# Kernel tuning notes

Measured on AMD Instinct MI355X. Metric: run time of the kernel, lower is better.

The kernel has to match this reference:

```python
import jax, jax.numpy as jnp
import numpy as np

BETA = 0.5
LAMBDA = 0.5
EPS = 1e-24


def setup_inputs() -> dict:
    key = jax.random.key(0)
    k1, k2 = jax.random.split(key)
    seq = jax.random.normal(k1, (32, 512, 128), dtype=jnp.float32)
    fism_items = jax.random.normal(k2, (32, 2048, 128), dtype=jnp.float32)
    return {"seq": seq, "fism_items": fism_items}


def reference(seq, fism_items):
    # scores: [B, L, N]
    w = jnp.einsum('bld,bnd->bln', seq, fism_items)
    w_shift = w - jnp.max(w, axis=-1, keepdims=True)
    exp_w = jnp.exp(w_shift)
    exp_sum = jnp.sum(exp_w, axis=-1, keepdims=True)
    if BETA != 1.0:
        exp_sum = jnp.power(exp_sum, jnp.float32(BETA))
    att = exp_w / (exp_sum + EPS)  # power-normalized softmax
    att_vecs = jnp.einsum('bln,bnd->bld', att, fism_items)
    if LAMBDA < 1:
        return seq * (1.0 - LAMBDA) + seq * att_vecs * LAMBDA
    return seq * att_vecs
```

## Files before the change

kernel.cpp:

```cpp
#include <hip/hip_runtime.h>
#include <hip/hip_bf16.h>
#include <math.h>

typedef _Float16 half8  __attribute__((ext_vector_type(8)));
typedef _Float16 half4v __attribute__((ext_vector_type(4)));
typedef __fp16   fp16x2 __attribute__((ext_vector_type(2)));
typedef float    f32x4  __attribute__((ext_vector_type(4)));
typedef float    f32x16 __attribute__((ext_vector_type(16)));
typedef int      i32x2v __attribute__((ext_vector_type(2)));

#define DDIM 128
#define LQ   512
#define NKV  2048
#define NB   32
#define NIT  16

union U32H2 { unsigned u; fp16x2 h; };
union PW    { unsigned u[4]; half8 h; };

__device__ __forceinline__ float xmax64(float v) {
  i32x2v r = __builtin_amdgcn_permlane32_swap(__float_as_int(v), __float_as_int(v), false, false);
  return fmaxf(__int_as_float(r[0]), __int_as_float(r[1]));
}
__device__ __forceinline__ float xsum64(float v) {
  i32x2v r = __builtin_amdgcn_permlane32_swap(__float_as_int(v), __float_as_int(v), false, false);
  return __int_as_float(r[0]) + __int_as_float(r[1]);
}

__device__ __forceinline__ void dma16(const void* g, void* l) {
  __builtin_amdgcn_global_load_lds(
      (const __attribute__((address_space(1))) unsigned int*)g,
      (__attribute__((address_space(3))) unsigned int*)l, 16, 0, 0);
}

__global__ __launch_bounds__(256)
void prep(const float* __restrict__ fism, _Float16* __restrict__ K16,
          _Float16* __restrict__ VT16)
{
  __shared__ _Float16 T[64 * DDIM];
  const int tid = threadIdx.x;
  const int bb  = blockIdx.x >> 5;
  const int kv0 = (blockIdx.x & 31) * 64;
  {
    const int r  = tid >> 2;
    const int cq = tid & 3;
    const float* src = fism + ((size_t)(bb*NKV + kv0 + r) * DDIM + cq*32);
    _Float16*    kd  = K16  + ((size_t)(bb*NKV + kv0 + r) * DDIM + cq*32);
    float4 v[8];
    #pragma unroll
    for (int k = 0; k < 8; ++k) v[k] = ((const float4*)src)[k];
    _Float16 h[32];
    #pragma unroll
    for (int k = 0; k < 8; ++k) {
      h[4*k+0] = (_Float16)v[k].x; h[4*k+1] = (_Float16)v[k].y;
      h[4*k+2] = (_Float16)v[k].z; h[4*k+3] = (_Float16)v[k].w;
    }
    #pragma unroll
    for (int k = 0; k < 4; ++k) ((half8*)kd)[k] = *(half8*)&h[8*k];
    #pragma unroll
    for (int j = 0; j < 32; ++j) {
      const int d = cq*32 + j;
      T[d*64 + (((r>>3) ^ (d&7))<<3) + (r&7)] = h[j];
    }
  }
  __syncthreads();
  {
    const int d  = tid >> 1;
    const int kh = tid & 1;
    _Float16* vd = VT16 + ((size_t)(bb*DDIM + d) * NKV + kv0 + kh*32);
    #pragma unroll
    for (int u = 0; u < 4; ++u) {
      const int k8 = kh*4 + u;
      ((half8*)vd)[u] = *(half8*)&T[d*64 + ((k8 ^ (d&7))<<3)];
    }
  }
}

__global__ __launch_bounds__(256, 2)
void gattn(const float* __restrict__ seq, const _Float16* __restrict__ K16,
           const _Float16* __restrict__ VT16, float* __restrict__ out)
{
  __shared__ __align__(16) unsigned char POOL[65536];
  __shared__ float stats[2][32][4];

  const int tid  = threadIdx.x;
  const int lane = tid & 63;
  const int wv   = tid >> 6;
  const int qg   = wv & 1;
  const int kvh  = wv >> 1;
  const int l31  = lane & 31;
  const int hi   = lane >> 5;

  const int swz = (blockIdx.x & 7) * 32 + (blockIdx.x >> 3);
  const int b   = swz >> 3;
  const int qb  = (swz & 7) * 64;

  const float* seqB = seq + (size_t)b * LQ * DDIM;
  float*       outB = out + (size_t)b * LQ * DDIM;
  const _Float16* K16b  = K16  + (size_t)b * NKV * DDIM;
  const _Float16* VT16b = VT16 + (size_t)b * DDIM * NKV;

  half8 qf[8];
  {
    const int qrow = qb + qg * 32 + l31;
    #pragma unroll
    for (int c = 0; c < 8; ++c) {
      const float* p = seqB + (size_t)qrow * DDIM + c * 16 + hi * 8;
      float4 a  = *(const float4*)p;
      float4 b2 = *(const float4*)(p + 4);
      half8 h;
      h[0]=(_Float16)a.x;  h[1]=(_Float16)a.y;  h[2]=(_Float16)a.z;  h[3]=(_Float16)a.w;
      h[4]=(_Float16)b2.x; h[5]=(_Float16)b2.y; h[6]=(_Float16)b2.z; h[7]=(_Float16)b2.w;
      qf[c] = h;
    }
  }

  const bool isK = (wv < 2);
  const int  hst = isK ? wv : (wv - 2);
  int off[16];
  #pragma unroll
  for (int i = 0; i < 16; ++i) {
    const int unit = i*64 + lane;
    const int r16 = unit >> 4, sp = unit & 15;
    const int s = sp ^ (r16 & 15);
    if (isK) {
      off[i] = r16*128 + s*8;
    } else {
      const int d = r16*2 + (s >> 3);
      off[i] = d*2048 + (s & 7)*8;
    }
  }
  const _Float16* sb0 = isK ? (K16b + (size_t)hst*1024*128) : (VT16b + hst*1024);
  const int tstr  = isK ? 8192 : 64;
  const int lbase = (isK ? 0 : 32768) + hst*16384;

  auto stage = [&](int tt) {
    const _Float16* s0 = sb0 + (size_t)tt * tstr;
    #pragma unroll
    for (int i = 0; i < 16; ++i)
      dma16(s0 + off[i], &POOL[lbase + i*1024]);
  };

  f32x16 acc[4];
  #pragma unroll
  for (int dt = 0; dt < 4; ++dt)
    #pragma unroll
    for (int i = 0; i < 16; ++i) acc[dt][i] = 0.f;

  float m_run = -INFINITY, tmax = -INFINITY, S_run = 0.f;

  stage(0);

  for (int t = 0; t < NIT; ++t) {
    __syncthreads();

    f32x16 sv[2];
    __builtin_amdgcn_s_setprio(1);
    #pragma unroll
    for (int ns = 0; ns < 2; ++ns) {
      f32x16 x;
      #pragma unroll
      for (int i = 0; i < 16; ++i) x[i] = 0.f;
      const int krow = ns*32 + l31;
      const int kb_  = kvh*16384 + krow*256;
      const int ksw  = krow & 15;
      #pragma unroll
      for (int c = 0; c < 8; ++c) {
        const int u = 2*c + hi;
        half8 ka = *(const half8*)&POOL[kb_ + ((u ^ ksw) << 4)];
        x = __builtin_amdgcn_mfma_f32_32x32x16_f16(ka, qf[c], x, 0, 0, 0);
      }
      sv[ns] = x;
    }
    __builtin_amdgcn_s_setprio(0);

    __syncthreads();
    if (isK && t + 1 < NIT) stage(t + 1);

    float mx[16];
    #pragma unroll
    for (int i = 0; i < 16; ++i) mx[i] = fmaxf(sv[0][i], sv[1][i]);
    #pragma unroll
    for (int st = 8; st > 0; st >>= 1)
      #pragma unroll
      for (int i = 0; i < st; ++i) mx[i] = fmaxf(mx[i], mx[i+st]);
    const float cmax = xmax64(mx[0]);
    tmax = fmaxf(tmax, cmax);
    if (__any(cmax > m_run + 8.f)) {
      const float mn = fmaxf(m_run, cmax);
      const float sc = __expf(m_run - mn);
      S_run *= sc;
      m_run = mn;
      #pragma unroll
      for (int dt = 0; dt < 4; ++dt) acc[dt] *= sc;
    }
    float ts[16];
    #pragma unroll
    for (int i = 0; i < 16; ++i) {
      const float p0 = __expf(sv[0][i] - m_run);
      const float p1 = __expf(sv[1][i] - m_run);
      sv[0][i] = p0; sv[1][i] = p1;
      ts[i] = p0 + p1;
    }
    #pragma unroll
    for (int st = 8; st > 0; st >>= 1)
      #pragma unroll
      for (int i = 0; i < st; ++i) ts[i] += ts[i+st];
    S_run += xsum64(ts[0]);

    PW pw[4];
    #pragma unroll
    for (int nss = 0; nss < 2; ++nss)
      #pragma unroll
      for (int b0 = 0; b0 < 2; ++b0) {
        U32H2 t0, t1, t2, t3;
        t0.h = __builtin_amdgcn_cvt_pkrtz(sv[nss][8*b0+0], sv[nss][8*b0+1]);
        t1.h = __builtin_amdgcn_cvt_pkrtz(sv[nss][8*b0+2], sv[nss][8*b0+3]);
        t2.h = __builtin_amdgcn_cvt_pkrtz(sv[nss][8*b0+4], sv[nss][8*b0+5]);
        t3.h = __builtin_amdgcn_cvt_pkrtz(sv[nss][8*b0+6], sv[nss][8*b0+7]);
        i32x2v r0 = __builtin_amdgcn_permlane32_swap((int)t0.u, (int)t2.u, false, false);
        i32x2v r1 = __builtin_amdgcn_permlane32_swap((int)t1.u, (int)t3.u, false, false);
        const int kb = 2*nss + b0;
        pw[kb].u[0] = (unsigned)r0[0];
        pw[kb].u[1] = (unsigned)r1[0];
        pw[kb].u[2] = (unsigned)r0[1];
        pw[kb].u[3] = (unsigned)r1[1];
      }

    __builtin_amdgcn_s_setprio(1);
    #pragma unroll
    for (int dt = 0; dt < 4; ++dt) {
      const int d    = dt*32 + l31;
      const int dRow = d >> 1, dSub = d & 1;
      const int vsw  = dRow & 15;
      const int vb   = 32768 + kvh*16384 + dRow*256;
      #pragma unroll
      for (int kb = 0; kb < 4; ++kb) {
        const int u = dSub*8 + kb*2 + hi;
        half8 vtf = *(const half8*)&POOL[vb + ((u ^ vsw) << 4)];
        acc[dt] = __builtin_amdgcn_mfma_f32_32x32x16_f16(vtf, pw[kb].h, acc[dt], 0, 0, 0);
      }
    }
    __builtin_amdgcn_s_setprio(0);

    __syncthreads();
    if (!isK && t + 1 < NIT) stage(t + 1);
  }

  __syncthreads();

  if (kvh == 1) {
    float* base = (float*)&POOL[qg * 16384];
    #pragma unroll
    for (int dt = 0; dt < 4; ++dt)
      #pragma unroll
      for (int rg = 0; rg < 4; ++rg) {
        const int j = dt*4 + rg;
        f32x4 v = {acc[dt][4*rg+0], acc[dt][4*rg+1], acc[dt][4*rg+2], acc[dt][4*rg+3]};
        *(f32x4*)&base[lane*64 + ((j ^ (lane & 15)) << 2)] = v;
      }
    if (lane < 32) {
      stats[qg][lane][0] = m_run;
      stats[qg][lane][1] = S_run;
      stats[qg][lane][2] = tmax;
    }
  }
  __syncthreads();

  if (kvh == 0) {
    const float m1 = stats[qg][l31][0];
    const float S1 = stats[qg][l31][1];
    const float t1 = stats[qg][l31][2];
    const float M2 = fmaxf(m_run, m1);
    const float e0 = __expf(m_run - M2), e1 = __expf(m1 - M2);
    const float S  = S_run * e0 + S1 * e1;
    const float T  = fmaxf(tmax, t1);
    const float fs = __expf(0.5f * (M2 - T)) * rsqrtf(S);

    const float* base = (const float*)&POOL[qg * 16384];
    const int qrw = qb + qg*32 + l31;
    #pragma unroll
    for (int dt = 0; dt < 4; ++dt) {
      #pragma unroll
      for (int rg = 0; rg < 4; ++rg) {
        const int j = dt*4 + rg;
        const f32x4 pj = *(const f32x4*)&base[lane*64 + ((j ^ (lane & 15)) << 2)];
        f32x4 av;
        #pragma unroll
        for (int i = 0; i < 4; ++i)
          av[i] = (acc[dt][4*rg+i] * e0 + pj[i] * e1) * fs;
        const int d0 = dt*32 + rg*8 + hi*4;
        const float4 s = *(const float4*)&seqB[(size_t)qrw * DDIM + d0];
        float4 o;
        o.x = 0.5f * s.x * (1.f + av[0]);
        o.y = 0.5f * s.y * (1.f + av[1]);
        o.z = 0.5f * s.z * (1.f + av[2]);
        o.w = 0.5f * s.w * (1.f + av[3]);
        *(float4*)&outB[(size_t)qrw * DDIM + d0] = o;
      }
    }
  }
}

__global__ __launch_bounds__(512, 2)
void gattn_fb(const float* __restrict__ seq, const float* __restrict__ fism,
              float* __restrict__ out)
{
  const int tid  = threadIdx.x;
  const int lane = tid & 63;
  const int wv   = tid >> 6;
  const int wq   = wv & 1;
  const int kvq  = wv >> 1;
  const int l31  = lane & 31;
  const int hi   = lane >> 5;

  const int swz = (blockIdx.x & 7) * 32 + (blockIdx.x >> 3);
  const int b   = swz >> 3;
  const int qb  = (swz & 7) * 64;

  const float* seqB = seq  + (size_t)b * LQ * DDIM;
  const float* fisB = fism + (size_t)b * NKV * DDIM;
  float*       outB = out  + (size_t)b * LQ * DDIM;

  __shared__ _Float16 Ksh[4][64 * DDIM];
  __shared__ _Float16 VTsh[4][(DDIM/2) * 128];
  __shared__ float    stats[4][2][32][3];

  half8 qf[8];
  {
    const int qrow = qb + wq * 32 + l31;
    #pragma unroll
    for (int c = 0; c < 8; ++c) {
      const float* p = seqB + (size_t)qrow * DDIM + c * 16 + hi * 8;
      float4 a  = *(const float4*)p;
      float4 b2 = *(const float4*)(p + 4);
      half8 h;
      h[0]=(_Float16)a.x;  h[1]=(_Float16)a.y;  h[2]=(_Float16)a.z;  h[3]=(_Float16)a.w;
      h[4]=(_Float16)b2.x; h[5]=(_Float16)b2.y; h[6]=(_Float16)b2.z; h[7]=(_Float16)b2.w;
      qf[c] = h;
    }
  }

  const int sp   = tid >> 3;
  const int dgrp = tid & 7;
  const int qstg = sp >> 4;
  const int spc  = sp & 15;

  f32x16 acc[4];
  #pragma unroll
  for (int dt = 0; dt < 4; ++dt)
    #pragma unroll
    for (int i = 0; i < 16; ++i) acc[dt][i] = 0.f;

  float m_run = -INFINITY, tmax = -INFINITY, S_run = 0.f;

  auto write_stage = [&](const float4* v) {
    #pragma unroll
    for (int r = 0; r < 4; ++r) {
      const int row = 4*spc + r;
      #pragma unroll
      for (int hh = 0; hh < 2; ++hh) {
        const float4 x = v[r*4 + hh*2];
        const float4 y = v[r*4 + hh*2 + 1];
        half8 h;
        h[0]=(_Float16)x.x; h[1]=(_Float16)x.y; h[2]=(_Float16)x.z; h[3]=(_Float16)x.w;
        h[4]=(_Float16)y.x; h[5]=(_Float16)y.y; h[6]=(_Float16)y.z; h[7]=(_Float16)y.w;
        const int idx = row*DDIM + ((dgrp*16 + hh*8) ^ (8*(row & 15)));
        *(half8*)&Ksh[qstg][idx] = h;
      }
    }
    #pragma unroll
    for (int k = 0; k < 16; ++k) {
      const int d = dgrp*16 + k;
      const int dRow = d >> 1, dSub = d & 1;
      half4v pk;
      #pragma unroll
      for (int r = 0; r < 4; ++r)
        pk[r] = (_Float16)(((const float*)&v[r*4 + (k>>2)])[k&3]);
      const int idx = dRow*128 + ((dSub*64 + 4*spc) ^ (8*(dRow & 15)));
      *(half4v*)&VTsh[qstg][idx] = pk;
    }
  };

  auto load_glb = [&](float4* v, int t) {
    const float* src = fisB + (size_t)(qstg*(NKV/4) + t*64) * DDIM;
    #pragma unroll
    for (int r = 0; r < 4; ++r)
      #pragma unroll
      for (int k = 0; k < 4; ++k)
        v[r*4+k] = *(const float4*)(src + (size_t)(4*spc + r)*DDIM + dgrp*16 + k*4);
  };

  {
    float4 stg[16];
    load_glb(stg, 0);
    write_stage(stg);
  }

  for (int t = 0; t < 8; ++t) {
    __syncthreads();
    float4 nxt[16];
    const bool have = (t + 1 < 8);
    if (have) load_glb(nxt, t + 1);

    f32x16 sv[2];
    #pragma unroll
    for (int nss = 0; nss < 2; ++nss) {
      f32x16 x;
      #pragma unroll
      for (int i = 0; i < 16; ++i) x[i] = 0.f;
      const int row = nss*32 + l31;
      const int sw  = 8*(row & 15);
      #pragma unroll
      for (int c = 0; c < 8; ++c) {
        const int idx = row*DDIM + ((c*16 + hi*8) ^ sw);
        half8 kf = *(const half8*)&Ksh[kvq][idx];
        x = __builtin_amdgcn_mfma_f32_32x32x16_f16(kf, qf[c], x, 0, 0, 0);
      }
      sv[nss] = x;
    }

    float mx[16];
    #pragma unroll
    for (int i = 0; i < 16; ++i) mx[i] = fmaxf(sv[0][i], sv[1][i]);
    #pragma unroll
    for (int st = 8; st > 0; st >>= 1)
      #pragma unroll
      for (int i = 0; i < st; ++i) mx[i] = fmaxf(mx[i], mx[i+st]);
    const float cmax = xmax64(mx[0]);
    tmax = fmaxf(tmax, cmax);
    if (__any(cmax > m_run + 8.f)) {
      const float mn = fmaxf(m_run, cmax);
      const float sc = __expf(m_run - mn);
      S_run *= sc;
      m_run = mn;
      #pragma unroll
      for (int dt = 0; dt < 4; ++dt) acc[dt] *= sc;
    }
    float ts[16];
    #pragma unroll
    for (int i = 0; i < 16; ++i) {
      const float p0 = __expf(sv[0][i] - m_run);
      const float p1 = __expf(sv[1][i] - m_run);
      sv[0][i] = p0; sv[1][i] = p1;
      ts[i] = p0 + p1;
    }
    #pragma unroll
    for (int st = 8; st > 0; st >>= 1)
      #pragma unroll
      for (int i = 0; i < st; ++i) ts[i] += ts[i+st];
    S_run += xsum64(ts[0]);

    PW pw[4];
    #pragma unroll
    for (int nss = 0; nss < 2; ++nss)
      #pragma unroll
      for (int b0 = 0; b0 < 2; ++b0) {
        U32H2 t0, t1, t2, t3;
        t0.h = __builtin_amdgcn_cvt_pkrtz(sv[nss][8*b0+0], sv[nss][8*b0+1]);
        t1.h = __builtin_amdgcn_cvt_pkrtz(sv[nss][8*b0+2], sv[nss][8*b0+3]);
        t2.h = __builtin_amdgcn_cvt_pkrtz(sv[nss][8*b0+4], sv[nss][8*b0+5]);
        t3.h = __builtin_amdgcn_cvt_pkrtz(sv[nss][8*b0+6], sv[nss][8*b0+7]);
        i32x2v r0 = __builtin_amdgcn_permlane32_swap((int)t0.u, (int)t2.u, false, false);
        i32x2v r1 = __builtin_amdgcn_permlane32_swap((int)t1.u, (int)t3.u, false, false);
        const int kb = 2*nss + b0;
        pw[kb].u[0] = (unsigned)r0[0];
        pw[kb].u[1] = (unsigned)r1[0];
        pw[kb].u[2] = (unsigned)r0[1];
        pw[kb].u[3] = (unsigned)r1[1];
      }

    #pragma unroll
    for (int dt = 0; dt < 4; ++dt) {
      const int d    = dt*32 + l31;
      const int dRow = d >> 1, dSub = d & 1;
      const int sw   = 8*(dRow & 15);
      #pragma unroll
      for (int kb = 0; kb < 4; ++kb) {
        const int idx = dRow*128 + ((dSub*64 + kb*16 + hi*8) ^ sw);
        half8 vtf = *(const half8*)&VTsh[kvq][idx];
        acc[dt] = __builtin_amdgcn_mfma_f32_32x32x16_f16(vtf, pw[kb].h, acc[dt], 0, 0, 0);
      }
    }

    __syncthreads();
    if (have) write_stage(nxt);
  }

  __syncthreads();

  float* Kf  = (float*)&Ksh[0][0];
  float* VTf = (float*)&VTsh[0][0];
  if (kvq != 0) {
    const int rgn = (kvq - 1) * 2 + wq;
    float* base = (rgn < 4) ? (Kf + rgn * 4096) : (VTf + (rgn - 4) * 4096);
    #pragma unroll
    for (int dt = 0; dt < 4; ++dt)
      #pragma unroll
      for (int rg = 0; rg < 4; ++rg) {
        f32x4 v = {acc[dt][4*rg+0], acc[dt][4*rg+1], acc[dt][4*rg+2], acc[dt][4*rg+3]};
        *(f32x4*)&base[lane*64 + (((dt*4+rg) ^ (lane & 15)) * 4)] = v;
      }
    if (lane < 32) {
      stats[kvq][wq][lane][0] = m_run;
      stats[kvq][wq][lane][1] = S_run;
      stats[kvq][wq][lane][2] = tmax;
    }
  }
  __syncthreads();

  if (kvq == 0) {
    float mj[4], Sj[4], tj[4];
    mj[0] = m_run; Sj[0] = S_run; tj[0] = tmax;
    #pragma unroll
    for (int j = 1; j < 4; ++j) {
      mj[j] = stats[j][wq][l31][0];
      Sj[j] = stats[j][wq][l31][1];
      tj[j] = stats[j][wq][l31][2];
    }
    const float M = fmaxf(fmaxf(tj[0], tj[1]), fmaxf(tj[2], tj[3]));
    float fj[4], den = 0.f;
    #pragma unroll
    for (int j = 0; j < 4; ++j) { fj[j] = __expf(mj[j] - M); den += fj[j] * Sj[j]; }
    const float rs = rsqrtf(den);
    #pragma unroll
    for (int j = 0; j < 4; ++j) fj[j] *= rs;

    const int qrow = qb + wq*32 + l31;
    #pragma unroll
    for (int dt = 0; dt < 4; ++dt) {
      #pragma unroll
      for (int rg = 0; rg < 4; ++rg) {
        f32x4 av = {acc[dt][4*rg+0], acc[dt][4*rg+1], acc[dt][4*rg+2], acc[dt][4*rg+3]};
        av *= fj[0];
        #pragma unroll
        for (int j = 1; j < 4; ++j) {
          const int rgn = (j - 1) * 2 + wq;
          const float* base = (rgn < 4) ? (Kf + rgn * 4096) : (VTf + (rgn - 4) * 4096);
          const f32x4 pj = *(const f32x4*)&base[lane*64 + (((dt*4+rg) ^ (lane & 15)) * 4)];
          av += pj * fj[j];
        }
        const int d0 = dt*32 + rg*8 + hi*4;
        const float4 s = *(const float4*)&seqB[(size_t)qrow * DDIM + d0];
        float4 o;
        o.x = 0.5f * s.x * (1.f + av[0]);
        o.y = 0.5f * s.y * (1.f + av[1]);
        o.z = 0.5f * s.z * (1.f + av[2]);
        o.w = 0.5f * s.w * (1.f + av[3]);
        *(float4*)&outB[(size_t)qrow * DDIM + d0] = o;
      }
    }
  }
}

extern "C" void kernel_launch(void* const* d_in, const int* in_sizes, int n_in,
                              void* d_out, int out_size, void* d_ws, size_t ws_size,
                              hipStream_t stream) {
  const float* seq  = (const float*)d_in[0];
  const float* fism = (const float*)d_in[1];
  float* out = (float*)d_out;
  if (ws_size >= 33554432ull) {
    _Float16* K16  = (_Float16*)d_ws;
    _Float16* VT16 = K16 + (size_t)NB * NKV * DDIM;
    prep<<<dim3(1024), dim3(256), 0, stream>>>(fism, K16, VT16);
    gattn<<<dim3(256), dim3(256), 0, stream>>>(seq, K16, VT16, out);
  } else {
    gattn_fb<<<dim3(256), dim3(512), 0, stream>>>(seq, fism, out);
  }
}
```

Baseline: 60.75 us.

## Load MFMA-fragment-ordered K/V directly to registers, split KV across four waves

The prep kernel now writes K and V in the exact per-lane MFMA fragment order, so the attention kernel loads them straight from global memory into registers instead of staging through LDS with DMA and block barriers. Each block handles 32 queries, with its four waves each covering a quarter of the KV range, and the grid doubles to 512 blocks. The four partial softmax states are merged at the end through shared memory. This removes the per-iteration __syncthreads and LDS traffic, at the cost of much higher register pressure from holding K and V fragments in registers, and each block now re-reads K/V for only 32 queries.

```diff
diff --git a/kernel.cpp b/kernel.cpp
--- a/kernel.cpp
+++ b/kernel.cpp
@@ -13,7 +13,7 @@
 #define LQ   512
 #define NKV  2048
 #define NB   32
-#define NIT  16
+#define NIT  8
 
 union U32H2 { unsigned u; fp16x2 h; };
 union PW    { unsigned u[4]; half8 h; };
@@ -27,25 +27,19 @@
   return __int_as_float(r[0]) + __int_as_float(r[1]);
 }
 
-__device__ __forceinline__ void dma16(const void* g, void* l) {
-  __builtin_amdgcn_global_load_lds(
-      (const __attribute__((address_space(1))) unsigned int*)g,
-      (__attribute__((address_space(3))) unsigned int*)l, 16, 0, 0);
-}
-
 __global__ __launch_bounds__(256)
-void prep(const float* __restrict__ fism, _Float16* __restrict__ K16,
-          _Float16* __restrict__ VT16)
+void prep(const float* __restrict__ fism, _Float16* __restrict__ KF,
+          _Float16* __restrict__ VF)
 {
   __shared__ _Float16 T[64 * DDIM];
   const int tid = threadIdx.x;
   const int bb  = blockIdx.x >> 5;
-  const int kv0 = (blockIdx.x & 31) * 64;
+  const int idx = blockIdx.x & 31;
+  const int kv0 = idx * 64;
   {
     const int r  = tid >> 2;
     const int cq = tid & 3;
     const float* src = fism + ((size_t)(bb*NKV + kv0 + r) * DDIM + cq*32);
-    _Float16*    kd  = K16  + ((size_t)(bb*NKV + kv0 + r) * DDIM + cq*32);
     float4 v[8];
     #pragma unroll
     for (int k = 0; k < 8; ++k) v[k] = ((const float4*)src)[k];
@@ -55,8 +49,15 @@
       h[4*k+0] = (_Float16)v[k].x; h[4*k+1] = (_Float16)v[k].y;
       h[4*k+2] = (_Float16)v[k].z; h[4*k+3] = (_Float16)v[k].w;
     }
-    #pragma unroll
-    for (int k = 0; k < 4; ++k) ((half8*)kd)[k] = *(half8*)&h[8*k];
+    const size_t kfb = (size_t)(bb*32 + idx) * 8192;
+    const int ns = r >> 5, l31r = r & 31;
+    #pragma unroll
+    for (int g = 0; g < 4; ++g) {
+      const int c   = cq*2 + (g >> 1);
+      const int hig = g & 1;
+      const int unit = (ns*8 + c)*64 + hig*32 + l31r;
+      *(half8*)&KF[kfb + (size_t)unit*8] = *(half8*)&h[(g>>1)*16 + hig*8];
+    }
     #pragma unroll
     for (int j = 0; j < 32; ++j) {
       const int d = cq*32 + j;
@@ -65,81 +66,53 @@
   }
   __syncthreads();
   {
-    const int d  = tid >> 1;
-    const int kh = tid & 1;
-    _Float16* vd = VT16 + ((size_t)(bb*DDIM + d) * NKV + kv0 + kh*32);
-    #pragma unroll
-    for (int u = 0; u < 4; ++u) {
-      const int k8 = kh*4 + u;
-      ((half8*)vd)[u] = *(half8*)&T[d*64 + ((k8 ^ (d&7))<<3)];
+    const size_t vfb = (size_t)(bb*32 + idx) * 8192;
+    #pragma unroll
+    for (int j = 0; j < 4; ++j) {
+      const int u  = tid*4 + j;
+      const int dt = u >> 8, kb = (u >> 6) & 3, l = u & 63;
+      const int d  = dt*32 + (l & 31);
+      const int kv8 = kb*2 + (l >> 5);
+      *(half8*)&VF[vfb + (size_t)u*8] = *(half8*)&T[d*64 + ((kv8 ^ (d & 7)) << 3)];
     }
   }
 }
 
 __global__ __launch_bounds__(256, 2)
-void gattn(const float* __restrict__ seq, const _Float16* __restrict__ K16,
-           const _Float16* __restrict__ VT16, float* __restrict__ out)
+void gattn(const float* __restrict__ seq, const _Float16* __restrict__ KF,
+           const _Float16* __restrict__ VF, float* __restrict__ out)
 {
-  __shared__ __align__(16) unsigned char POOL[65536];
-  __shared__ float stats[2][32][4];
+  __shared__ __align__(16) unsigned char POOL[49152];
+  __shared__ float stats[4][32][4];
 
   const int tid  = threadIdx.x;
   const int lane = tid & 63;
-  const int wv   = tid >> 6;
-  const int qg   = wv & 1;
-  const int kvh  = wv >> 1;
+  const int kvh  = tid >> 6;
   const int l31  = lane & 31;
   const int hi   = lane >> 5;
 
-  const int swz = (blockIdx.x & 7) * 32 + (blockIdx.x >> 3);
-  const int b   = swz >> 3;
-  const int qb  = (swz & 7) * 64;
+  const int swzb = (blockIdx.x & 7) * 64 + (blockIdx.x >> 3);
+  const int b    = swzb >> 4;
+  const int qb   = (swzb & 15) * 32;
 
   const float* seqB = seq + (size_t)b * LQ * DDIM;
   float*       outB = out + (size_t)b * LQ * DDIM;
-  const _Float16* K16b  = K16  + (size_t)b * NKV * DDIM;
-  const _Float16* VT16b = VT16 + (size_t)b * DDIM * NKV;
-
-  half8 qf[8];
-  {
-    const int qrow = qb + qg * 32 + l31;
-    #pragma unroll
-    for (int c = 0; c < 8; ++c) {
-      const float* p = seqB + (size_t)qrow * DDIM + c * 16 + hi * 8;
-      float4 a  = *(const float4*)p;
-      float4 b2 = *(const float4*)(p + 4);
-      half8 h;
-      h[0]=(_Float16)a.x;  h[1]=(_Float16)a.y;  h[2]=(_Float16)a.z;  h[3]=(_Float16)a.w;
-      h[4]=(_Float16)b2.x; h[5]=(_Float16)b2.y; h[6]=(_Float16)b2.z; h[7]=(_Float16)b2.w;
-      qf[c] = h;
-    }
-  }
-
-  const bool isK = (wv < 2);
-  const int  hst = isK ? wv : (wv - 2);
-  int off[16];
+
   #pragma unroll
-  for (int i = 0; i < 16; ++i) {
-    const int unit = i*64 + lane;
-    const int r16 = unit >> 4, sp = unit & 15;
-    const int s = sp ^ (r16 & 15);
-    if (isK) {
-      off[i] = r16*128 + s*8;
-    } else {
-      const int d = r16*2 + (s >> 3);
-      off[i] = d*2048 + (s & 7)*8;
-    }
-  }
-  const _Float16* sb0 = isK ? (K16b + (size_t)hst*1024*128) : (VT16b + hst*1024);
-  const int tstr  = isK ? 8192 : 64;
-  const int lbase = (isK ? 0 : 32768) + hst*16384;
-
-  auto stage = [&](int tt) {
-    const _Float16* s0 = sb0 + (size_t)tt * tstr;
-    #pragma unroll
-    for (int i = 0; i < 16; ++i)
-      dma16(s0 + off[i], &POOL[lbase + i*1024]);
-  };
+  for (int j = 0; j < 2; ++j) {
+    const int u = tid*2 + j;
+    const int c = u >> 6, l = u & 63;
+    const float* qs = seqB + (size_t)(qb + (l & 31)) * DDIM + c*16 + (l >> 5)*8;
+    float4 a  = ((const float4*)qs)[0];
+    float4 b2 = ((const float4*)qs)[1];
+    _Float16 hq[8];
+    hq[0]=(_Float16)a.x;  hq[1]=(_Float16)a.y;  hq[2]=(_Float16)a.z;  hq[3]=(_Float16)a.w;
+    hq[4]=(_Float16)b2.x; hq[5]=(_Float16)b2.y; hq[6]=(_Float16)b2.z; hq[7]=(_Float16)b2.w;
+    *(half8*)&POOL[u*16] = *(half8*)hq;
+  }
+  __syncthreads();
+
+  const int cb = b*32 + kvh*8;
 
   f32x16 acc[4];
   #pragma unroll
@@ -149,10 +122,22 @@
 
   float m_run = -INFINITY, tmax = -INFINITY, S_run = 0.f;
 
-  stage(0);
-
+  half8 kf[16], vfr0[8], vfr1[8];
+  {
+    const _Float16* KFc = KF + (size_t)cb * 8192;
+    #pragma unroll
+    for (int i = 0; i < 16; ++i) kf[i] = *(const half8*)(KFc + (size_t)(i*64 + lane)*8);
+  }
+
+  #pragma unroll
   for (int t = 0; t < NIT; ++t) {
-    __syncthreads();
+    const _Float16* VFc = VF + (size_t)(cb + t) * 8192;
+    #pragma unroll
+    for (int i = 0; i < 8; ++i) vfr0[i] = *(const half8*)(VFc + (size_t)(i*64 + lane)*8);
+
+    half8 qa[8];
+    #pragma unroll
+    for (int c = 0; c < 8; ++c) qa[c] = *(const half8*)&POOL[(c*64 + lane)*16];
 
     f32x16 sv[2];
     __builtin_amdgcn_s_setprio(1);
@@ -161,21 +146,20 @@
       f32x16 x;
       #pragma unroll
       for (int i = 0; i < 16; ++i) x[i] = 0.f;
-      const int krow = ns*32 + l31;
-      const int kb_  = kvh*16384 + krow*256;
-      const int ksw  = krow & 15;
-      #pragma unroll
-      for (int c = 0; c < 8; ++c) {
-        const int u = 2*c + hi;
-        half8 ka = *(const half8*)&POOL[kb_ + ((u ^ ksw) << 4)];
-        x = __builtin_amdgcn_mfma_f32_32x32x16_f16(ka, qf[c], x, 0, 0, 0);
-      }
+      #pragma unroll
+      for (int c = 0; c < 8; ++c)
+        x = __builtin_amdgcn_mfma_f32_32x32x16_f16(kf[ns*8+c], qa[c], x, 0, 0, 0);
       sv[ns] = x;
     }
     __builtin_amdgcn_s_setprio(0);
 
-    __syncthreads();
-    if (isK && t + 1 < NIT) stage(t + 1);
+    if (t + 1 < NIT) {
+      const _Float16* KFn = KF + (size_t)(cb + t + 1) * 8192;
+      #pragma unroll
+      for (int i = 0; i < 16; ++i) kf[i] = *(const half8*)(KFn + (size_t)(i*64 + lane)*8);
+    }
+    #pragma unroll
+    for (int i = 0; i < 8; ++i) vfr1[i] = *(const half8*)(VFc + (size_t)((8+i)*64 + lane)*8);
 
     float mx[16];
     #pragma unroll
@@ -230,27 +214,18 @@
     __builtin_amdgcn_s_setprio(1);
     #pragma unroll
     for (int dt = 0; dt < 4; ++dt) {
-      const int d    = dt*32 + l31;
-      const int dRow = d >> 1, dSub = d & 1;
-      const int vsw  = dRow & 15;
-      const int vb   = 32768 + kvh*16384 + dRow*256;
       #pragma unroll
       for (int kb = 0; kb < 4; ++kb) {
-        const int u = dSub*8 + kb*2 + hi;
-        half8 vtf = *(const half8*)&POOL[vb + ((u ^ vsw) << 4)];
-        acc[dt] = __builtin_amdgcn_mfma_f32_32x32x16_f16(vtf, pw[kb].h, acc[dt], 0, 0, 0);
+        const half8 v = (dt < 2) ? vfr0[dt*4 + kb] : vfr1[(dt-2)*4 + kb];
+        acc[dt] = __builtin_amdgcn_mfma_f32_32x32x16_f16(v, pw[kb].h, acc[dt], 0, 0, 0);
       }
     }
     __builtin_amdgcn_s_setprio(0);
-
-    __syncthreads();
-    if (!isK && t + 1 < NIT) stage(t + 1);
   }
 
   __syncthreads();
-
-  if (kvh == 1) {
-    float* base = (float*)&POOL[qg * 16384];
+  if (kvh != 0) {
+    float* base = (float*)&POOL[(kvh - 1) * 16384];
     #pragma unroll
     for (int dt = 0; dt < 4; ++dt)
       #pragma unroll
@@ -260,35 +235,46 @@
         *(f32x4*)&base[lane*64 + ((j ^ (lane & 15)) << 2)] = v;
       }
     if (lane < 32) {
-      stats[qg][lane][0] = m_run;
-      stats[qg][lane][1] = S_run;
-      stats[qg][lane][2] = tmax;
+      stats[kvh][lane][0] = m_run;
+      stats[kvh][lane][1] = S_run;
+      stats[kvh][lane][2] = tmax;
     }
   }
   __syncthreads();
 
   if (kvh == 0) {
-    const float m1 = stats[qg][l31][0];
-    const float S1 = stats[qg][l31][1];
-    const float t1 = stats[qg][l31][2];
-    const float M2 = fmaxf(m_run, m1);
-    const float e0 = __expf(m_run - M2), e1 = __expf(m1 - M2);
-    const float S  = S_run * e0 + S1 * e1;
-    const float T  = fmaxf(tmax, t1);
-    const float fs = __expf(0.5f * (M2 - T)) * rsqrtf(S);
-
-    const float* base = (const float*)&POOL[qg * 16384];
-    const int qrw = qb + qg*32 + l31;
+    float mj[4], Sj[4], tj[4];
+    mj[0] = m_run; Sj[0] = S_run; tj[0] = tmax;
+    #pragma unroll
+    for (int j = 1; j < 4; ++j) {
+      mj[j] = stats[j][l31][0];
+      Sj[j] = stats[j][l31][1];
+      tj[j] = stats[j][l31][2];
+    }
+    const float M = fmaxf(fmaxf(mj[0], mj[1]), fmaxf(mj[2], mj[3]));
+    const float T = fmaxf(fmaxf(tj[0], tj[1]), fmaxf(tj[2], tj[3]));
+    float ej[4], den = 0.f;
+    #pragma unroll
+    for (int j = 0; j < 4; ++j) { ej[j] = __expf(mj[j] - M); den += ej[j] * Sj[j]; }
+    const float fs = __expf(0.5f * (M - T)) * rsqrtf(den);
+    #pragma unroll
+    for (int j = 0; j < 4; ++j) ej[j] *= fs;
+
+    const int qrw = qb + l31;
     #pragma unroll
     for (int dt = 0; dt < 4; ++dt) {
       #pragma unroll
       for (int rg = 0; rg < 4; ++rg) {
-        const int j = dt*4 + rg;
-        const f32x4 pj = *(const f32x4*)&base[lane*64 + ((j ^ (lane & 15)) << 2)];
+        const int jj = dt*4 + rg;
         f32x4 av;
         #pragma unroll
-        for (int i = 0; i < 4; ++i)
-          av[i] = (acc[dt][4*rg+i] * e0 + pj[i] * e1) * fs;
+        for (int i = 0; i < 4; ++i) av[i] = acc[dt][4*rg+i] * ej[0];
+        #pragma unroll
+        for (int j = 1; j < 4; ++j) {
+          const float* base = (const float*)&POOL[(j - 1) * 16384];
+          const f32x4 pj = *(const f32x4*)&base[lane*64 + ((jj ^ (lane & 15)) << 2)];
+          av += pj * ej[j];
+        }
         const int d0 = dt*32 + rg*8 + hi*4;
         const float4 s = *(const float4*)&seqB[(size_t)qrw * DDIM + d0];
         float4 o;
@@ -560,10 +546,10 @@
   const float* fism = (const float*)d_in[1];
   float* out = (float*)d_out;
   if (ws_size >= 33554432ull) {
-    _Float16* K16  = (_Float16*)d_ws;
-    _Float16* VT16 = K16 + (size_t)NB * NKV * DDIM;
-    prep<<<dim3(1024), dim3(256), 0, stream>>>(fism, K16, VT16);
-    gattn<<<dim3(256), dim3(256), 0, stream>>>(seq, K16, VT16, out);
+    _Float16* KF = (_Float16*)d_ws;
+    _Float16* VF = KF + (size_t)NB * NKV * DDIM;
+    prep<<<dim3(1024), dim3(256), 0, stream>>>(fism, KF, VF);
+    gattn<<<dim3(512), dim3(256), 0, stream>>>(seq, KF, VF, out);
   } else {
     gattn_fb<<<dim3(256), dim3(512), 0, stream>>>(seq, fism, out);
   }
```

New measurement: 62.54 us. 2.9% more time.

## Pre-swizzle K/V into MFMA fragment order and double-buffer LDS stages

Applied to the files above, without the earlier changes.

The prep kernel now writes K and V^T in exactly the per-lane MFMA fragment order, so the attention kernel's DMA loads become contiguous and its LDS reads need no XOR swizzle arithmetic. LDS grows to 128 KB to double-buffer each KV tile, so the next stage is issued right after a single barrier per iteration instead of two barriers with split K/V staging. In exchange occupancy drops from two blocks per CU to one, and the linear fragment layout may cause LDS bank conflicts on the ds_read side.

```diff
diff --git a/kernel.cpp b/kernel.cpp
--- a/kernel.cpp
+++ b/kernel.cpp
@@ -34,18 +34,18 @@
 }
 
 __global__ __launch_bounds__(256)
-void prep(const float* __restrict__ fism, _Float16* __restrict__ K16,
-          _Float16* __restrict__ VT16)
+void prep(const float* __restrict__ fism, _Float16* __restrict__ KF,
+          _Float16* __restrict__ VF)
 {
   __shared__ _Float16 T[64 * DDIM];
   const int tid = threadIdx.x;
   const int bb  = blockIdx.x >> 5;
-  const int kv0 = (blockIdx.x & 31) * 64;
+  const int idx = blockIdx.x & 31;
+  const int kv0 = idx * 64;
   {
     const int r  = tid >> 2;
     const int cq = tid & 3;
     const float* src = fism + ((size_t)(bb*NKV + kv0 + r) * DDIM + cq*32);
-    _Float16*    kd  = K16  + ((size_t)(bb*NKV + kv0 + r) * DDIM + cq*32);
     float4 v[8];
     #pragma unroll
     for (int k = 0; k < 8; ++k) v[k] = ((const float4*)src)[k];
@@ -55,8 +55,15 @@
       h[4*k+0] = (_Float16)v[k].x; h[4*k+1] = (_Float16)v[k].y;
       h[4*k+2] = (_Float16)v[k].z; h[4*k+3] = (_Float16)v[k].w;
     }
-    #pragma unroll
-    for (int k = 0; k < 4; ++k) ((half8*)kd)[k] = *(half8*)&h[8*k];
+    const size_t kfb = (size_t)(bb*32 + idx) * 8192;
+    const int ns = r >> 5, l31r = r & 31;
+    #pragma unroll
+    for (int g = 0; g < 4; ++g) {
+      const int c   = cq*2 + (g >> 1);
+      const int hig = g & 1;
+      const int unit = (ns*8 + c)*64 + hig*32 + l31r;
+      *(half8*)&KF[kfb + (size_t)unit*8] = *(half8*)&h[(g>>1)*16 + hig*8];
+    }
     #pragma unroll
     for (int j = 0; j < 32; ++j) {
       const int d = cq*32 + j;
@@ -65,22 +72,23 @@
   }
   __syncthreads();
   {
-    const int d  = tid >> 1;
-    const int kh = tid & 1;
-    _Float16* vd = VT16 + ((size_t)(bb*DDIM + d) * NKV + kv0 + kh*32);
-    #pragma unroll
-    for (int u = 0; u < 4; ++u) {
-      const int k8 = kh*4 + u;
-      ((half8*)vd)[u] = *(half8*)&T[d*64 + ((k8 ^ (d&7))<<3)];
-    }
-  }
-}
-
-__global__ __launch_bounds__(256, 2)
-void gattn(const float* __restrict__ seq, const _Float16* __restrict__ K16,
-           const _Float16* __restrict__ VT16, float* __restrict__ out)
+    const size_t vfb = (size_t)(bb*32 + idx) * 8192;
+    #pragma unroll
+    for (int j = 0; j < 4; ++j) {
+      const int u  = tid*4 + j;
+      const int dt = u >> 8, kb = (u >> 6) & 3, l = u & 63;
+      const int d  = dt*32 + (l & 31);
+      const int kv8 = kb*2 + (l >> 5);
+      *(half8*)&VF[vfb + (size_t)u*8] = *(half8*)&T[d*64 + ((kv8 ^ (d & 7)) << 3)];
+    }
+  }
+}
+
+__global__ __launch_bounds__(256, 1)
+void gattn(const float* __restrict__ seq, const _Float16* __restrict__ KF,
+           const _Float16* __restrict__ VF, float* __restrict__ out)
 {
-  __shared__ __align__(16) unsigned char POOL[65536];
+  __shared__ __align__(16) unsigned char POOL[131072];
   __shared__ float stats[2][32][4];
 
   const int tid  = threadIdx.x;
@@ -97,8 +105,23 @@
 
   const float* seqB = seq + (size_t)b * LQ * DDIM;
   float*       outB = out + (size_t)b * LQ * DDIM;
-  const _Float16* K16b  = K16  + (size_t)b * NKV * DDIM;
-  const _Float16* VT16b = VT16 + (size_t)b * DDIM * NKV;
+  const _Float16* KFb = KF + (size_t)b * 32 * 8192;
+  const _Float16* VFb = VF + (size_t)b * 32 * 8192;
+
+  const bool isK = (wv < 2);
+  const int  hst = isK ? wv : (wv - 2);
+  const _Float16* sbase = (isK ? KFb : VFb) + (size_t)hst * 16 * 8192;
+  const int lgrp = (isK ? 0 : 65536) + hst * 32768;
+
+  auto stage = [&](int tt) {
+    const _Float16* s0 = sbase + (size_t)tt * 8192;
+    const int l0 = lgrp + (tt & 1) * 16384;
+    #pragma unroll
+    for (int i = 0; i < 16; ++i)
+      dma16(s0 + (size_t)(i*64 + lane)*8, &POOL[l0 + i*1024]);
+  };
+
+  stage(0);
 
   half8 qf[8];
   {
@@ -115,32 +138,6 @@
     }
   }
 
-  const bool isK = (wv < 2);
-  const int  hst = isK ? wv : (wv - 2);
-  int off[16];
-  #pragma unroll
-  for (int i = 0; i < 16; ++i) {
-    const int unit = i*64 + lane;
-    const int r16 = unit >> 4, sp = unit & 15;
-    const int s = sp ^ (r16 & 15);
-    if (isK) {
-      off[i] = r16*128 + s*8;
-    } else {
-      const int d = r16*2 + (s >> 3);
-      off[i] = d*2048 + (s & 7)*8;
-    }
-  }
-  const _Float16* sb0 = isK ? (K16b + (size_t)hst*1024*128) : (VT16b + hst*1024);
-  const int tstr  = isK ? 8192 : 64;
-  const int lbase = (isK ? 0 : 32768) + hst*16384;
-
-  auto stage = [&](int tt) {
-    const _Float16* s0 = sb0 + (size_t)tt * tstr;
-    #pragma unroll
-    for (int i = 0; i < 16; ++i)
-      dma16(s0 + off[i], &POOL[lbase + i*1024]);
-  };
-
   f32x16 acc[4];
   #pragma unroll
   for (int dt = 0; dt < 4; ++dt)
@@ -149,10 +146,12 @@
 
   float m_run = -INFINITY, tmax = -INFINITY, S_run = 0.f;
 
-  stage(0);
-
   for (int t = 0; t < NIT; ++t) {
     __syncthreads();
+    if (t + 1 < NIT) stage(t + 1);
+
+    const int kbB = kvh*32768 + (t & 1)*16384;
+    const int vbB = 65536 + kvh*32768 + (t & 1)*16384;
 
     f32x16 sv[2];
     __builtin_amdgcn_s_setprio(1);
@@ -161,21 +160,14 @@
       f32x16 x;
       #pragma unroll
       for (int i = 0; i < 16; ++i) x[i] = 0.f;
-      const int krow = ns*32 + l31;
-      const int kb_  = kvh*16384 + krow*256;
-      const int ksw  = krow & 15;
       #pragma unroll
       for (int c = 0; c < 8; ++c) {
-        const int u = 2*c + hi;
-        half8 ka = *(const half8*)&POOL[kb_ + ((u ^ ksw) << 4)];
+        half8 ka = *(const half8*)&POOL[kbB + ((ns*8 + c)*64 + lane)*16];
         x = __builtin_amdgcn_mfma_f32_32x32x16_f16(ka, qf[c], x, 0, 0, 0);
       }
       sv[ns] = x;
     }
     __builtin_amdgcn_s_setprio(0);
-
-    __syncthreads();
-    if (isK && t + 1 < NIT) stage(t + 1);
 
     float mx[16];
     #pragma unroll
@@ -230,21 +222,13 @@
     __builtin_amdgcn_s_setprio(1);
     #pragma unroll
     for (int dt = 0; dt < 4; ++dt) {
-      const int d    = dt*32 + l31;
-      const int dRow = d >> 1, dSub = d & 1;
-      const int vsw  = dRow & 15;
-      const int vb   = 32768 + kvh*16384 + dRow*256;
       #pragma unroll
       for (int kb = 0; kb < 4; ++kb) {
-        const int u = dSub*8 + kb*2 + hi;
-        half8 vtf = *(const half8*)&POOL[vb + ((u ^ vsw) << 4)];
+        half8 vtf = *(const half8*)&POOL[vbB + ((dt*4 + kb)*64 + lane)*16];
         acc[dt] = __builtin_amdgcn_mfma_f32_32x32x16_f16(vtf, pw[kb].h, acc[dt], 0, 0, 0);
       }
     }
     __builtin_amdgcn_s_setprio(0);
-
-    __syncthreads();
-    if (!isK && t + 1 < NIT) stage(t + 1);
   }
 
   __syncthreads();
@@ -560,10 +544,10 @@
   const float* fism = (const float*)d_in[1];
   float* out = (float*)d_out;
   if (ws_size >= 33554432ull) {
-    _Float16* K16  = (_Float16*)d_ws;
-    _Float16* VT16 = K16 + (size_t)NB * NKV * DDIM;
-    prep<<<dim3(1024), dim3(256), 0, stream>>>(fism, K16, VT16);
-    gattn<<<dim3(256), dim3(256), 0, stream>>>(seq, K16, VT16, out);
+    _Float16* KF = (_Float16*)d_ws;
+    _Float16* VF = KF + (size_t)NB * NKV * DDIM;
+    prep<<<dim3(1024), dim3(256), 0, stream>>>(fism, KF, VF);
+    gattn<<<dim3(256), dim3(256), 0, stream>>>(seq, KF, VF, out);
   } else {
     gattn_fb<<<dim3(256), dim3(512), 0, stream>>>(seq, fism, out);
   }
```

Result: no change. 60.53 us (-0.4%).
